# Optimization experiments

Hardware: AMD Instinct MI355X
Metric: run time of the kernel (lower is better)

Reference implementation:

```python
import jax, jax.numpy as jnp
import numpy as np

B, N, C, H, DEPTH = 64, 256, 384, 8, 6
HD = C // H  # 48
SCALE = HD ** -0.5
LN_EPS = 1e-5


def setup_inputs() -> dict:
    key = jax.random.key(0)
    ks = jax.random.split(key, 12)
    g = lambda k, shape, s=0.05: jax.random.normal(k, shape, jnp.float32) * s
    return {
        "x": jax.random.normal(ks[0], (B, N, 2), jnp.float32),
        "mask": jnp.zeros((B, N), jnp.float32),  # additive padding mask (0 = keep)
        "emb_w1": g(ks[1], (C, 2), 0.5),
        "emb_b1": jnp.zeros((C,), jnp.float32),
        "emb_w2": g(ks[2], (C, C)),
        "emb_b2": jnp.zeros((C,), jnp.float32),
        "qkv_w": g(ks[3], (DEPTH, 3 * C, C)),
        "proj_w": g(ks[4], (DEPTH, C, C)),
        "proj_b": jnp.zeros((DEPTH, C), jnp.float32),
        "mlp_w1": g(ks[5], (DEPTH, C, C)),
        "mlp_b1": jnp.zeros((DEPTH, C), jnp.float32),
        "mlp_w2": g(ks[6], (DEPTH, C, C)),
        "mlp_b2": jnp.zeros((DEPTH, C), jnp.float32),
        "ln1_s": jnp.ones((DEPTH, C), jnp.float32),
        "ln1_b": jnp.zeros((DEPTH, C), jnp.float32),
        "ln2_s": jnp.ones((DEPTH, C), jnp.float32),
        "ln2_b": jnp.zeros((DEPTH, C), jnp.float32),
    }


def _layernorm(x, s, b):
    mu = jnp.mean(x, axis=-1, keepdims=True)
    var = jnp.mean((x - mu) ** 2, axis=-1, keepdims=True)
    return (x - mu) * jax.lax.rsqrt(var + LN_EPS) * s + b


def _rope(t):
    # t: (B, H, N, HD); interleaved rotary, matching the torch module
    hd = t.shape[-1]
    inv_freq = 1.0 / (10000.0 ** (jnp.arange(0, hd, 2, dtype=jnp.float32) / hd))
    pos = jnp.arange(t.shape[2], dtype=jnp.float32)
    f = pos[:, None] * inv_freq[None, :]            # (N, HD/2)
    cos, sin = jnp.cos(f), jnp.sin(f)
    xu, xe = t[..., 0::2], t[..., 1::2]
    ru = xu * cos - xe * sin
    re = xu * sin + xe * cos
    return jnp.stack([ru, re], axis=-1).reshape(t.shape)


def reference(x, mask, emb_w1, emb_b1, emb_w2, emb_b2, qkv_w, proj_w, proj_b,
              mlp_w1, mlp_b1, mlp_w2, mlp_b2, ln1_s, ln1_b, ln2_s, ln2_b):
    # BallEmbedding: Linear -> ReLU -> Linear
    h = jax.nn.relu(x @ emb_w1.T + emb_b1) @ emb_w2.T + emb_b2  # (B, N, C)
    for i in range(DEPTH):
        # pre-norm rotary attention
        y = _layernorm(h, ln1_s[i], ln1_b[i])
        qkv = (y @ qkv_w[i].T).reshape(B, N, 3, H, HD).transpose(2, 0, 3, 1, 4)
        q, k, v = qkv[0], qkv[1], qkv[2]                      # (B, H, N, HD)
        q = _rope(q) * SCALE
        k = _rope(k)
        attn = jnp.einsum('bhqd,bhkd->bhqk', q, k)
        attn = attn + mask[:, None, None, :] + mask[:, None, :, None]
        attn = jax.nn.softmax(attn, axis=-1)
        o = jnp.einsum('bhqk,bhkd->bhqd', attn, v)
        o = o.transpose(0, 2, 1, 3).reshape(B, N, C)
        h = h + (o @ proj_w[i].T + proj_b[i])
        # pre-norm MLP (hidden = dim, ReLU)
        y = _layernorm(h, ln2_s[i], ln2_b[i])
        m = jax.nn.relu(y @ mlp_w1[i].T + mlp_b1[i]) @ mlp_w2[i].T + mlp_b2[i]
        h = h + m
    return h
```

## Files before the change

kernel.cpp:

```cpp
#include <hip/hip_runtime.h>
#include <hip/hip_bf16.h>
#include <math.h>

#define BATCH 64
#define SEQ   256
#define CH    384
#define NHEAD 8
#define HD    48
#define DEPTH 6
#define NTOK  (BATCH*SEQ)
#define C3    (3*CH)
#define LN_EPS 1e-5f
#define ATT_SCALE 0.14433756729740643f

typedef __attribute__((ext_vector_type(8)))  short bf16x8;
typedef __attribute__((ext_vector_type(4)))  float f32x4;
typedef __attribute__((ext_vector_type(16))) float f32x16;

__device__ __forceinline__ ushort f2bf(float f) {
    __hip_bfloat16 h = __float2bfloat16(f);
    return *(ushort*)&h;
}
__device__ __forceinline__ float bfu2f(ushort u) {
    uint t = ((uint)u) << 16;
    union { uint u; float f; } c; c.u = t; return c.f;
}
__device__ __forceinline__ uint pk2(float a, float b) {
    return (uint)f2bf(a) | ((uint)f2bf(b) << 16);
}

#define AS1(p) ((const __attribute__((address_space(1))) void*)(p))
#define AS3(p) ((__attribute__((address_space(3))) void*)(uintptr_t)(p))
#define WAITVMC(N) asm volatile("s_waitcnt vmcnt(" #N ")" ::: "memory")
#define TAILSYNC() do { \
    asm volatile("s_waitcnt lgkmcnt(0)" ::: "memory"); \
    __builtin_amdgcn_sched_barrier(0); \
    __builtin_amdgcn_s_barrier(); } while (0)

__global__ void zero_kernel(float4* __restrict__ p) {
    p[blockIdx.x*256 + threadIdx.x] = float4{0.f,0.f,0.f,0.f};
}

__global__ void f2bf4_kernel(const float* __restrict__ in, ushort* __restrict__ out) {
    int i = (blockIdx.x*256 + threadIdx.x)*4;
    float4 v = *(const float4*)(in + i);
    ushort4 o;
    o.x = f2bf(v.x); o.y = f2bf(v.y); o.z = f2bf(v.z); o.w = f2bf(v.w);
    *(ushort4*)(out + i) = o;
}

__global__ void rope_table_kernel(float2* __restrict__ tbl) {
    int pos = threadIdx.x;
    for (int j = 0; j < 24; ++j) {
        float freq = exp2f(-(float)j * (13.287712379549449f / 24.0f));
        float ang = (float)pos * freq;
        float s, c;
        sincosf(ang, &s, &c);
        tbl[pos*24 + j] = make_float2(c, s);
    }
}

__global__ void embed1_kernel(const float* __restrict__ x, const float* __restrict__ w1,
                              const float* __restrict__ b1, ushort* __restrict__ out) {
    int idx = blockIdx.x*256 + threadIdx.x;
    int m = idx / CH, c = idx - m*CH;
    float v = x[m*2]*w1[c*2] + x[m*2+1]*w1[c*2+1] + b1[c];
    out[idx] = f2bf(fmaxf(v, 0.f));
}

__global__ __launch_bounds__(256) void prep_kernel(
        const float* __restrict__ Wsrc, const float* __restrict__ gam,
        const float* __restrict__ bet, const float* __restrict__ bias,
        int npl, ushort* __restrict__ Wdst, float2* __restrict__ uvout) {
    int rr   = blockIdx.x*4 + (threadIdx.x >> 6);
    int lane = threadIdx.x & 63;
    int layer = rr / npl;
    const float* wp = Wsrc + (size_t)rr*CH;
    const float* gp = gam + layer*CH;
    const float* bp = bet + layer*CH;
    float u = 0.f, vv = 0.f;
    if (lane < 48) {
        int c0 = lane*8;
        float w8[8];
        *(float4*)&w8[0] = *(const float4*)(wp + c0);
        *(float4*)&w8[4] = *(const float4*)(wp + c0 + 4);
        union { ushort us[8]; bf16x8 v; } o;
        #pragma unroll
        for (int j = 0; j < 8; ++j) {
            float wg = w8[j] * gp[c0+j];
            u  += wg;
            vv += bp[c0+j] * w8[j];
            o.us[j] = f2bf(wg);
        }
        *(bf16x8*)(Wdst + (size_t)rr*CH + c0) = o.v;
    }
    #pragma unroll
    for (int o = 1; o < 64; o <<= 1) { u += __shfl_xor(u, o); vv += __shfl_xor(vv, o); }
    if (lane == 0) {
        if (bias) vv += bias[rr];
        uvout[rr] = make_float2(u, vv);
    }
}

template<bool LNAFF, bool RELU, bool RESID, bool QKV>
__global__ __launch_bounds__(256) void gemm_kernel(
        const ushort* __restrict__ A,
        const ushort* __restrict__ W,
        const float*  __restrict__ bias,
        const float2* __restrict__ uv,
        const float2* __restrict__ sbr,
        const float*  __restrict__ resid,
        float*  __restrict__ hout,
        ushort* __restrict__ bout,
        int ldo,
        float2* __restrict__ sbw,
        ushort* __restrict__ vtbuf) {
    __shared__ __align__(16) ushort As[2][8192];
    __shared__ __align__(16) ushort Bs[2][8192];
    const int tid  = threadIdx.x;
    const int lane = tid & 63;
    const int w    = tid >> 6;
    const int l15  = lane & 15;
    const int g    = lane >> 4;
    const int wr   = (w >> 1) * 64;
    const int wc   = (w & 1) * 64;
    const int m0   = blockIdx.y * 128;
    const int n0   = blockIdx.x * 128;

    const int srow = lane >> 3;
    const int scol = ((lane & 7) ^ srow) * 8;
    auto stage = [&](int pb, int t) {
        int k0 = t*64;
        #pragma unroll
        for (int c = 0; c < 8; ++c) {
            int chunk = w + c*4;
            if (chunk < 16) {
                const ushort* gp = A + (size_t)(m0 + chunk*8 + srow)*CH + k0 + scol;
                __builtin_amdgcn_global_load_lds(AS1(gp), AS3(&As[pb][chunk*512]), 16, 0, 0);
            } else {
                const ushort* gp = W + (size_t)(n0 + (chunk-16)*8 + srow)*CH + k0 + scol;
                __builtin_amdgcn_global_load_lds(AS1(gp), AS3(&Bs[pb][(chunk-16)*512]), 16, 0, 0);
            }
        }
    };

    f32x4 acc[4][4] = {};
    const int xm = (l15 & 7) << 4;

    stage(0, 0);
    for (int t = 0; t < 6; ++t) {
        if (t + 1 < 6) stage((t+1)&1, t+1);
        if (t < 5) { WAITVMC(8); } else { WAITVMC(0); }
        __builtin_amdgcn_s_barrier();
        const int pb = t & 1;
        #pragma unroll
        for (int kk = 0; kk < 2; ++kk) {
            bf16x8 a[4], b[4];
            #pragma unroll
            for (int i = 0; i < 4; ++i)
                a[i] = *(const bf16x8*)((const char*)As[pb]
                        + (wr + i*16 + l15)*128 + ((kk*64 + 16*g) ^ xm));
            #pragma unroll
            for (int j = 0; j < 4; ++j)
                b[j] = *(const bf16x8*)((const char*)Bs[pb]
                        + (wc + j*16 + l15)*128 + ((kk*64 + 16*g) ^ xm));
            #pragma unroll
            for (int i = 0; i < 4; ++i)
                #pragma unroll
                for (int j = 0; j < 4; ++j)
                    acc[i][j] = __builtin_amdgcn_mfma_f32_16x16x32_bf16(a[i], b[j], acc[i][j], 0, 0, 0);
        }
        TAILSYNC();
    }

    const int cbase = n0 + wc + l15;
    const int rbase = m0 + wr + g*4;
    if (LNAFF) {
        float2 uvv[4];
        #pragma unroll
        for (int j = 0; j < 4; ++j) uvv[j] = uv[cbase + j*16];
        const bool isV = QKV && (n0 >= 2*CH);
        int hj[4], dj[4];
        if (isV) {
            #pragma unroll
            for (int j = 0; j < 4; ++j) {
                int nn = cbase + j*16 - 2*CH;
                hj[j] = nn / HD; dj[j] = nn - hj[j]*HD;
            }
        }
        #pragma unroll
        for (int i = 0; i < 4; ++i) {
            float muv[4], invv[4];
            #pragma unroll
            for (int r = 0; r < 4; ++r) {
                float2 s2 = sbr[rbase + i*16 + r];
                float mu = s2.x * (1.0f/CH);
                float var = s2.y * (1.0f/CH) - mu*mu;
                muv[r] = mu; invv[r] = rsqrtf(var + LN_EPS);
            }
            if (isV) {
                int bb   = rbase >> 8;
                int seq0 = (rbase + i*16) & 255;
                #pragma unroll
                for (int j = 0; j < 4; ++j) {
                    float vr[4];
                    #pragma unroll
                    for (int r = 0; r < 4; ++r)
                        vr[r] = invv[r]*(acc[i][j][r] - muv[r]*uvv[j].x) + uvv[j].y;
                    uint2 val;
                    val.x = pk2(vr[0], vr[1]);
                    val.y = pk2(vr[2], vr[3]);
                    *(uint2*)(vtbuf + (((size_t)bb*NHEAD + hj[j])*HD + dj[j])*SEQ + seq0) = val;
                }
            } else {
                #pragma unroll
                for (int r = 0; r < 4; ++r) {
                    int m = rbase + i*16 + r;
                    #pragma unroll
                    for (int j = 0; j < 4; ++j) {
                        float v = invv[r]*(acc[i][j][r] - muv[r]*uvv[j].x) + uvv[j].y;
                        if (RELU) v = fmaxf(v, 0.f);
                        bout[(size_t)m*ldo + cbase + j*16] = f2bf(v);
                    }
                }
            }
        }
    } else {
        float bj[4];
        #pragma unroll
        for (int j = 0; j < 4; ++j) bj[j] = bias[cbase + j*16];
        #pragma unroll
        for (int i = 0; i < 4; ++i)
            #pragma unroll
            for (int r = 0; r < 4; ++r) {
                int m = rbase + i*16 + r;
                #pragma unroll
                for (int j = 0; j < 4; ++j) {
                    int n = cbase + j*16;
                    float v = acc[i][j][r] + bj[j];
                    if (RESID) v += resid[(size_t)m*CH + n];
                    acc[i][j][r] = v;
                    hout[(size_t)m*CH + n] = v;
                    bout[(size_t)m*CH + n] = f2bf(v);
                }
            }
        if (sbw) {
            #pragma unroll
            for (int i = 0; i < 4; ++i)
                #pragma unroll
                for (int r = 0; r < 4; ++r) {
                    float s = 0.f, q = 0.f;
                    #pragma unroll
                    for (int j = 0; j < 4; ++j) {
                        float v = acc[i][j][r];
                        s += v; q += v*v;
                    }
                    #pragma unroll
                    for (int off = 1; off < 16; off <<= 1) {
                        s += __shfl_xor(s, off);
                        q += __shfl_xor(q, off);
                    }
                    if (l15 == 0) {
                        int m = rbase + i*16 + r;
                        atomicAdd(&sbw[m].x, s);
                        atomicAdd(&sbw[m].y, q);
                    }
                }
        }
    }
}

__global__ __launch_bounds__(512) void attn_kernel(
        const ushort* __restrict__ qkv, const ushort* __restrict__ vtbuf,
        const float* __restrict__ mask,
        const float2* __restrict__ tbl, ushort* __restrict__ obuf) {
    __shared__ __align__(16) ushort Kf[8*3*64*8];
    __shared__ __align__(16) ushort Vf[2*16*64*8];
    __shared__ float Ms[SEQ];

    const int bid = blockIdx.x;
    const int b   = bid >> 3;
    const int hh  = bid & 7;
    const int tid = threadIdx.x;
    const int lane = tid & 63;
    const int hi   = (lane >> 5);
    const int q5   = lane & 31;
    const ushort* base = qkv + (size_t)b*SEQ*C3;

    {
        int t   = tid >> 6;
        int row = t*32 + q5;
        const ushort* kp = base + (size_t)row*C3 + CH + hh*HD;
        #pragma unroll
        for (int s = 0; s < 3; ++s) {
            union { ushort us[8]; bf16x8 v; } raw;
            raw.v = *(const bf16x8*)(kp + s*16 + hi*8);
            union { uint w[4]; bf16x8 v; } u;
            #pragma unroll
            for (int p = 0; p < 4; ++p) {
                float2 cs = tbl[row*24 + s*8 + hi*4 + p];
                float xu = bfu2f(raw.us[2*p]), xe = bfu2f(raw.us[2*p+1]);
                u.w[p] = pk2(xu*cs.x - xe*cs.y, xu*cs.y + xe*cs.x);
            }
            *(bf16x8*)&Kf[((t*3 + s)*64 + lane)*8] = u.v;
        }
    }
    {
        const ushort* vt = vtbuf + (size_t)(b*NHEAD + hh)*HD*SEQ;
        #pragma unroll
        for (int p = 0; p < 4; ++p) {
            int dt = p >> 1;
            int sp = (tid >> 6)*2 + (p & 1);
            int dd = dt*32 + q5;
            bf16x8 u = (bf16x8)(short)0;
            if (dd < HD) u = *(const bf16x8*)(vt + (size_t)dd*SEQ + sp*16 + hi*8);
            *(bf16x8*)&Vf[((dt*16 + sp)*64 + lane)*8] = u;
        }
    }
    if (tid < SEQ) Ms[tid] = mask[b*SEQ + tid];

    const int wv    = tid >> 6;
    const int qrow  = wv*32 + q5;
    bf16x8 qf[3];
    {
        const ushort* qp = base + (size_t)qrow*C3 + hh*HD;
        #pragma unroll
        for (int s = 0; s < 3; ++s) {
            union { ushort us[8]; bf16x8 v; } raw;
            raw.v = *(const bf16x8*)(qp + s*16 + hi*8);
            union { uint w[4]; bf16x8 v; } u;
            #pragma unroll
            for (int p = 0; p < 4; ++p) {
                float2 cs = tbl[qrow*24 + s*8 + hi*4 + p];
                float xu = bfu2f(raw.us[2*p]), xe = bfu2f(raw.us[2*p+1]);
                u.w[p] = pk2((xu*cs.x - xe*cs.y)*ATT_SCALE, (xu*cs.y + xe*cs.x)*ATT_SCALE);
            }
            qf[s] = u.v;
        }
    }
    __syncthreads();

    f32x16 st[8] = {};
    #pragma unroll
    for (int t = 0; t < 8; ++t)
        #pragma unroll
        for (int s = 0; s < 3; ++s) {
            bf16x8 af = *(const bf16x8*)&Kf[((t*3 + s)*64 + lane)*8];
            st[t] = __builtin_amdgcn_mfma_f32_32x32x16_bf16(af, qf[s], st[t], 0, 0, 0);
        }

    float mx = -1e30f;
    #pragma unroll
    for (int t = 0; t < 8; ++t)
        #pragma unroll
        for (int r = 0; r < 16; ++r) {
            int kt = t*32 + (r & 3) + 8*(r >> 2) + 4*hi;
            float s = st[t][r] + Ms[kt];
            st[t][r] = s;
            mx = fmaxf(mx, s);
        }
    mx = fmaxf(mx, __shfl_xor(mx, 32));
    float sum = 0.f;
    #pragma unroll
    for (int t = 0; t < 8; ++t)
        #pragma unroll
        for (int r = 0; r < 16; ++r) {
            float p = __expf(st[t][r] - mx);
            st[t][r] = p;
            sum += p;
        }
    sum += __shfl_xor(sum, 32);

    f32x16 oacc[2] = {};
    #pragma unroll
    for (int t = 0; t < 8; ++t) {
        uint w[4][2];
        #pragma unroll
        for (int g = 0; g < 4; ++g) {
            w[g][0] = pk2(st[t][g*4+0], st[t][g*4+1]);
            w[g][1] = pk2(st[t][g*4+2], st[t][g*4+3]);
        }
        #pragma unroll
        for (int o = 0; o < 2; ++o) {
            uint x0 = __shfl_xor(hi ? w[2*o][0] : w[2*o+1][0], 32);
            uint x1 = __shfl_xor(hi ? w[2*o][1] : w[2*o+1][1], 32);
            union { uint w[4]; bf16x8 v; } pf;
            if (hi == 0) { pf.w[0] = w[2*o][0]; pf.w[1] = w[2*o][1]; pf.w[2] = x0; pf.w[3] = x1; }
            else         { pf.w[0] = x0; pf.w[1] = x1; pf.w[2] = w[2*o+1][0]; pf.w[3] = w[2*o+1][1]; }
            int sp = t*2 + o;
            #pragma unroll
            for (int dt = 0; dt < 2; ++dt) {
                bf16x8 vf = *(const bf16x8*)&Vf[((dt*16 + sp)*64 + lane)*8];
                oacc[dt] = __builtin_amdgcn_mfma_f32_32x32x16_bf16(vf, pf.v, oacc[dt], 0, 0, 0);
            }
        }
    }

    float inv = 1.f / sum;
    ushort* op = obuf + ((size_t)(b*SEQ + qrow))*CH + hh*HD;
    #pragma unroll
    for (int dt = 0; dt < 2; ++dt)
        #pragma unroll
        for (int rg = 0; rg < 4; ++rg) {
            int d0 = dt*32 + rg*8 + hi*4;
            if (d0 < HD) {
                uint2 val;
                val.x = pk2(oacc[dt][rg*4+0]*inv, oacc[dt][rg*4+1]*inv);
                val.y = pk2(oacc[dt][rg*4+2]*inv, oacc[dt][rg*4+3]*inv);
                *(uint2*)(op + d0) = val;
            }
        }
}

extern "C" void kernel_launch(void* const* d_in, const int* in_sizes, int n_in,
                              void* d_out, int out_size, void* d_ws, size_t ws_size,
                              hipStream_t stream) {
    const float* x      = (const float*)d_in[0];
    const float* mask   = (const float*)d_in[1];
    const float* emb_w1 = (const float*)d_in[2];
    const float* emb_b1 = (const float*)d_in[3];
    const float* emb_w2 = (const float*)d_in[4];
    const float* emb_b2 = (const float*)d_in[5];
    const float* qkv_w  = (const float*)d_in[6];
    const float* proj_w = (const float*)d_in[7];
    const float* proj_b = (const float*)d_in[8];
    const float* mlp_w1 = (const float*)d_in[9];
    const float* mlp_b1 = (const float*)d_in[10];
    const float* mlp_w2 = (const float*)d_in[11];
    const float* mlp_b2 = (const float*)d_in[12];
    const float* ln1_s  = (const float*)d_in[13];
    const float* ln1_b  = (const float*)d_in[14];
    const float* ln2_s  = (const float*)d_in[15];
    const float* ln2_b  = (const float*)d_in[16];

    const size_t S1 = (size_t)NTOK*CH;
    float*  h     = (float*)d_ws;
    ushort* hbf   = (ushort*)(h + S1);
    ushort* qkvbf = hbf + S1;
    ushort* ybf   = qkvbf + 3*S1;
    ushort* t2bf  = ybf  + S1;
    ushort* obf   = t2bf + S1;
    ushort* vtbuf = obf  + S1;
    ushort* wb_emb2 = vtbuf + S1;
    ushort* wb_proj = wb_emb2 + 147456;
    ushort* wb_m2   = wb_proj + 884736;
    ushort* wqkvp   = wb_m2   + 884736;
    ushort* wm1p    = wqkvp   + 2654208;
    float2* uv_qkv  = (float2*)(wm1p + 884736);
    float2* uv_m1   = uv_qkv + 6912;
    float2* sb      = uv_m1  + 2304;
    float*  tbl     = (float*)(sb + 12*NTOK);

    dim3 gqkv(9, 128);
    dim3 g384(3, 128);

    zero_kernel<<<384, 256, 0, stream>>>((float4*)sb);
    rope_table_kernel<<<1, 256, 0, stream>>>((float2*)tbl);
    f2bf4_kernel<<<144, 256, 0, stream>>>(emb_w2, wb_emb2);
    f2bf4_kernel<<<864, 256, 0, stream>>>(proj_w, wb_proj);
    f2bf4_kernel<<<864, 256, 0, stream>>>(mlp_w2, wb_m2);
    prep_kernel<<<1728, 256, 0, stream>>>(qkv_w,  ln1_s, ln1_b, nullptr, C3, wqkvp, uv_qkv);
    prep_kernel<<<576,  256, 0, stream>>>(mlp_w1, ln2_s, ln2_b, mlp_b1,  CH, wm1p,  uv_m1);

    embed1_kernel<<<(NTOK*CH)/256, 256, 0, stream>>>(x, emb_w1, emb_b1, ybf);
    gemm_kernel<false,false,false,false><<<g384, 256, 0, stream>>>(ybf, wb_emb2, emb_b2,
            nullptr, nullptr, nullptr, h, hbf, CH, sb, nullptr);

    for (int i = 0; i < DEPTH; ++i) {
        gemm_kernel<true,false,false,true><<<gqkv, 256, 0, stream>>>(hbf,
                wqkvp + (size_t)i*C3*CH, nullptr, uv_qkv + i*C3, sb + (size_t)(2*i)*NTOK,
                nullptr, nullptr, qkvbf, C3, nullptr, vtbuf);
        attn_kernel<<<BATCH*NHEAD, 512, 0, stream>>>(qkvbf, vtbuf, mask,
                (const float2*)tbl, obf);
        gemm_kernel<false,false,true,false><<<g384, 256, 0, stream>>>(obf,
                wb_proj + (size_t)i*CH*CH, proj_b + i*CH, nullptr, nullptr,
                h, h, hbf, CH, sb + (size_t)(2*i+1)*NTOK, nullptr);
        gemm_kernel<true,true,false,false><<<g384, 256, 0, stream>>>(hbf,
                wm1p + (size_t)i*CH*CH, nullptr, uv_m1 + i*CH, sb + (size_t)(2*i+1)*NTOK,
                nullptr, nullptr, t2bf, CH, nullptr, nullptr);
        gemm_kernel<false,false,true,false><<<g384, 256, 0, stream>>>(t2bf,
                wb_m2 + (size_t)i*CH*CH, mlp_b2 + i*CH, nullptr, nullptr,
                h, h, hbf, CH, (i < DEPTH-1) ? (sb + (size_t)(2*i+2)*NTOK) : nullptr, nullptr);
    }
    hipMemcpyAsync(d_out, h, S1*sizeof(float), hipMemcpyDeviceToDevice, stream);
}
```

Before: 856.1 us.

## Fuse RoPE and scaling into QKV GEMM epilogue and swizzle GEMM block order

Applies the rotary embedding and the attention scale to Q and K inside the QKV GEMM epilogue, pairing even and odd columns with a lane shuffle. The attention kernel can then copy K and V straight into LDS with async global-to-LDS loads instead of decoding and rotating them in registers. The V-transpose buffer is padded to 64 rows per head so the V loads no longer need a bounds check. GEMM launches move to a 1D grid with a block-order swizzle meant to improve L2 reuse, at the cost of extra table loads and shuffles in the GEMM epilogue.

```diff
diff --git a/kernel.cpp b/kernel.cpp
--- a/kernel.cpp
+++ b/kernel.cpp
@@ -112,9 +112,10 @@
         const float*  __restrict__ resid,
         float*  __restrict__ hout,
         ushort* __restrict__ bout,
-        int ldo,
+        int ldo, int nx,
         float2* __restrict__ sbw,
-        ushort* __restrict__ vtbuf) {
+        ushort* __restrict__ vtbuf,
+        const float2* __restrict__ tbl) {
     __shared__ __align__(16) ushort As[2][8192];
     __shared__ __align__(16) ushort Bs[2][8192];
     const int tid  = threadIdx.x;
@@ -124,8 +125,10 @@
     const int g    = lane >> 4;
     const int wr   = (w >> 1) * 64;
     const int wc   = (w & 1) * 64;
-    const int m0   = blockIdx.y * 128;
-    const int n0   = blockIdx.x * 128;
+    const int lin  = blockIdx.x;
+    const int swz  = (lin & 7)*((int)gridDim.x >> 3) + (lin >> 3);
+    const int m0   = (swz / nx) * 128;
+    const int n0   = (swz % nx) * 128;
 
     const int srow = lane >> 3;
     const int scol = ((lane & 7) ^ srow) * 8;
@@ -179,13 +182,14 @@
         float2 uvv[4];
         #pragma unroll
         for (int j = 0; j < 4; ++j) uvv[j] = uv[cbase + j*16];
-        const bool isV = QKV && (n0 >= 2*CH);
-        int hj[4], dj[4];
-        if (isV) {
+        const int region = QKV ? (n0 / 384) : 0;
+        int hj[4], dj[4], jp[4];
+        if (QKV) {
             #pragma unroll
             for (int j = 0; j < 4; ++j) {
-                int nn = cbase + j*16 - 2*CH;
-                hj[j] = nn / HD; dj[j] = nn - hj[j]*HD;
+                int nn = cbase + j*16 - region*384;
+                if (region == 2) { hj[j] = nn / HD; dj[j] = nn - hj[j]*HD; }
+                else             { jp[j] = (nn % HD) >> 1; }
             }
         }
         #pragma unroll
@@ -198,7 +202,7 @@
                 float var = s2.y * (1.0f/CH) - mu*mu;
                 muv[r] = mu; invv[r] = rsqrtf(var + LN_EPS);
             }
-            if (isV) {
+            if (QKV && region == 2) {
                 int bb   = rbase >> 8;
                 int seq0 = (rbase + i*16) & 255;
                 #pragma unroll
@@ -210,15 +214,22 @@
                     uint2 val;
                     val.x = pk2(vr[0], vr[1]);
                     val.y = pk2(vr[2], vr[3]);
-                    *(uint2*)(vtbuf + (((size_t)bb*NHEAD + hj[j])*HD + dj[j])*SEQ + seq0) = val;
+                    *(uint2*)(vtbuf + (((size_t)bb*NHEAD + hj[j])*64 + dj[j])*SEQ + seq0) = val;
                 }
             } else {
                 #pragma unroll
                 for (int r = 0; r < 4; ++r) {
                     int m = rbase + i*16 + r;
+                    int pos = m & 255;
                     #pragma unroll
                     for (int j = 0; j < 4; ++j) {
                         float v = invv[r]*(acc[i][j][r] - muv[r]*uvv[j].x) + uvv[j].y;
+                        if (QKV) {
+                            float vx = __shfl_xor(v, 1);
+                            float2 cs = tbl[pos*24 + jp[j]];
+                            v = (l15 & 1) ? (vx*cs.y + v*cs.x) : (v*cs.x - vx*cs.y);
+                            if (region == 0) v *= ATT_SCALE;
+                        }
                         if (RELU) v = fmaxf(v, 0.f);
                         bout[(size_t)m*ldo + cbase + j*16] = f2bf(v);
                     }
@@ -272,8 +283,7 @@
 
 __global__ __launch_bounds__(512) void attn_kernel(
         const ushort* __restrict__ qkv, const ushort* __restrict__ vtbuf,
-        const float* __restrict__ mask,
-        const float2* __restrict__ tbl, ushort* __restrict__ obuf) {
+        const float* __restrict__ mask, ushort* __restrict__ obuf) {
     __shared__ __align__(16) ushort Kf[8*3*64*8];
     __shared__ __align__(16) ushort Vf[2*16*64*8];
     __shared__ float Ms[SEQ];
@@ -285,58 +295,35 @@
     const int lane = tid & 63;
     const int hi   = (lane >> 5);
     const int q5   = lane & 31;
+    const int twv  = tid >> 6;
     const ushort* base = qkv + (size_t)b*SEQ*C3;
 
     {
-        int t   = tid >> 6;
-        int row = t*32 + q5;
-        const ushort* kp = base + (size_t)row*C3 + CH + hh*HD;
-        #pragma unroll
-        for (int s = 0; s < 3; ++s) {
-            union { ushort us[8]; bf16x8 v; } raw;
-            raw.v = *(const bf16x8*)(kp + s*16 + hi*8);
-            union { uint w[4]; bf16x8 v; } u;
-            #pragma unroll
-            for (int p = 0; p < 4; ++p) {
-                float2 cs = tbl[row*24 + s*8 + hi*4 + p];
-                float xu = bfu2f(raw.us[2*p]), xe = bfu2f(raw.us[2*p+1]);
-                u.w[p] = pk2(xu*cs.x - xe*cs.y, xu*cs.y + xe*cs.x);
-            }
-            *(bf16x8*)&Kf[((t*3 + s)*64 + lane)*8] = u.v;
-        }
+        int row = twv*32 + q5;
+        const ushort* kp = base + (size_t)row*C3 + CH + hh*HD + hi*8;
+        #pragma unroll
+        for (int s = 0; s < 3; ++s)
+            __builtin_amdgcn_global_load_lds(AS1(kp + s*16), AS3(&Kf[(twv*3+s)*512]), 16, 0, 0);
     }
     {
-        const ushort* vt = vtbuf + (size_t)(b*NHEAD + hh)*HD*SEQ;
+        const ushort* vt = vtbuf + (size_t)(b*NHEAD + hh)*64*SEQ;
         #pragma unroll
         for (int p = 0; p < 4; ++p) {
             int dt = p >> 1;
-            int sp = (tid >> 6)*2 + (p & 1);
+            int sp = twv*2 + (p & 1);
             int dd = dt*32 + q5;
-            bf16x8 u = (bf16x8)(short)0;
-            if (dd < HD) u = *(const bf16x8*)(vt + (size_t)dd*SEQ + sp*16 + hi*8);
-            *(bf16x8*)&Vf[((dt*16 + sp)*64 + lane)*8] = u;
+            const ushort* vp = vt + (size_t)dd*SEQ + sp*16 + hi*8;
+            __builtin_amdgcn_global_load_lds(AS1(vp), AS3(&Vf[(dt*16+sp)*512]), 16, 0, 0);
         }
     }
     if (tid < SEQ) Ms[tid] = mask[b*SEQ + tid];
 
-    const int wv    = tid >> 6;
-    const int qrow  = wv*32 + q5;
+    const int qrow = twv*32 + q5;
     bf16x8 qf[3];
     {
-        const ushort* qp = base + (size_t)qrow*C3 + hh*HD;
-        #pragma unroll
-        for (int s = 0; s < 3; ++s) {
-            union { ushort us[8]; bf16x8 v; } raw;
-            raw.v = *(const bf16x8*)(qp + s*16 + hi*8);
-            union { uint w[4]; bf16x8 v; } u;
-            #pragma unroll
-            for (int p = 0; p < 4; ++p) {
-                float2 cs = tbl[qrow*24 + s*8 + hi*4 + p];
-                float xu = bfu2f(raw.us[2*p]), xe = bfu2f(raw.us[2*p+1]);
-                u.w[p] = pk2((xu*cs.x - xe*cs.y)*ATT_SCALE, (xu*cs.y + xe*cs.x)*ATT_SCALE);
-            }
-            qf[s] = u.v;
-        }
+        const ushort* qp = base + (size_t)qrow*C3 + hh*HD + hi*8;
+        #pragma unroll
+        for (int s = 0; s < 3; ++s) qf[s] = *(const bf16x8*)(qp + s*16);
     }
     __syncthreads();
 
@@ -441,7 +428,7 @@
     ushort* t2bf  = ybf  + S1;
     ushort* obf   = t2bf + S1;
     ushort* vtbuf = obf  + S1;
-    ushort* wb_emb2 = vtbuf + S1;
+    ushort* wb_emb2 = vtbuf + (size_t)BATCH*NHEAD*64*SEQ;
     ushort* wb_proj = wb_emb2 + 147456;
     ushort* wb_m2   = wb_proj + 884736;
     ushort* wqkvp   = wb_m2   + 884736;
@@ -450,9 +437,7 @@
     float2* uv_m1   = uv_qkv + 6912;
     float2* sb      = uv_m1  + 2304;
     float*  tbl     = (float*)(sb + 12*NTOK);
-
-    dim3 gqkv(9, 128);
-    dim3 g384(3, 128);
+    const float2* tblc = (const float2*)tbl;
 
     zero_kernel<<<384, 256, 0, stream>>>((float4*)sb);
     rope_table_kernel<<<1, 256, 0, stream>>>((float2*)tbl);
@@ -463,24 +448,24 @@
     prep_kernel<<<576,  256, 0, stream>>>(mlp_w1, ln2_s, ln2_b, mlp_b1,  CH, wm1p,  uv_m1);
 
     embed1_kernel<<<(NTOK*CH)/256, 256, 0, stream>>>(x, emb_w1, emb_b1, ybf);
-    gemm_kernel<false,false,false,false><<<g384, 256, 0, stream>>>(ybf, wb_emb2, emb_b2,
-            nullptr, nullptr, nullptr, h, hbf, CH, sb, nullptr);
+    gemm_kernel<false,false,false,false><<<384, 256, 0, stream>>>(ybf, wb_emb2, emb_b2,
+            nullptr, nullptr, nullptr, h, hbf, CH, 3, sb, nullptr, nullptr);
 
     for (int i = 0; i < DEPTH; ++i) {
-        gemm_kernel<true,false,false,true><<<gqkv, 256, 0, stream>>>(hbf,
+        gemm_kernel<true,false,false,true><<<1152, 256, 0, stream>>>(hbf,
                 wqkvp + (size_t)i*C3*CH, nullptr, uv_qkv + i*C3, sb + (size_t)(2*i)*NTOK,
-                nullptr, nullptr, qkvbf, C3, nullptr, vtbuf);
-        attn_kernel<<<BATCH*NHEAD, 512, 0, stream>>>(qkvbf, vtbuf, mask,
-                (const float2*)tbl, obf);
-        gemm_kernel<false,false,true,false><<<g384, 256, 0, stream>>>(obf,
+                nullptr, nullptr, qkvbf, C3, 9, nullptr, vtbuf, tblc);
+        attn_kernel<<<BATCH*NHEAD, 512, 0, stream>>>(qkvbf, vtbuf, mask, obf);
+        gemm_kernel<false,false,true,false><<<384, 256, 0, stream>>>(obf,
                 wb_proj + (size_t)i*CH*CH, proj_b + i*CH, nullptr, nullptr,
-                h, h, hbf, CH, sb + (size_t)(2*i+1)*NTOK, nullptr);
-        gemm_kernel<true,true,false,false><<<g384, 256, 0, stream>>>(hbf,
+                h, h, hbf, CH, 3, sb + (size_t)(2*i+1)*NTOK, nullptr, nullptr);
+        gemm_kernel<true,true,false,false><<<384, 256, 0, stream>>>(hbf,
                 wm1p + (size_t)i*CH*CH, nullptr, uv_m1 + i*CH, sb + (size_t)(2*i+1)*NTOK,
-                nullptr, nullptr, t2bf, CH, nullptr, nullptr);
-        gemm_kernel<false,false,true,false><<<g384, 256, 0, stream>>>(t2bf,
+                nullptr, nullptr, t2bf, CH, 3, nullptr, nullptr, nullptr);
+        gemm_kernel<false,false,true,false><<<384, 256, 0, stream>>>(t2bf,
                 wb_m2 + (size_t)i*CH*CH, mlp_b2 + i*CH, nullptr, nullptr,
-                h, h, hbf, CH, (i < DEPTH-1) ? (sb + (size_t)(2*i+2)*NTOK) : nullptr, nullptr);
+                h, h, hbf, CH, 3, (i < DEPTH-1) ? (sb + (size_t)(2*i+2)*NTOK) : nullptr,
+                nullptr, nullptr);
     }
     hipMemcpyAsync(d_out, h, S1*sizeof(float), hipMemcpyDeviceToDevice, stream);
 }
```

Measured after the change: 851.4 us. About the same (-0.6%).
